# Kernel tuning notes

Hardware: AMD Instinct MI355X
Metric: run time of the kernel (lower is better)

## Reference

```python
import jax, jax.numpy as jnp
import numpy as np

DIM = 1024
HEADS = 16
DIM_HEAD = 64
NB_FEATURES = 266
EPS = 1e-4


def _gaussian_orthogonal_random_matrix(nb_rows, nb_cols, seed=0):
    # Blocks of orthogonal rows (QR of gaussian), rows rescaled by gaussian row norms (scaling=0).
    rng = np.random.default_rng(seed)
    blocks = []
    full, rem = divmod(nb_rows, nb_cols)
    for _ in range(full):
        g = rng.standard_normal((nb_cols, nb_cols))
        q, _ = np.linalg.qr(g)
        blocks.append(q.T)
    if rem > 0:
        g = rng.standard_normal((nb_cols, nb_cols))
        q, _ = np.linalg.qr(g)
        blocks.append(q.T[:rem])
    mat = np.concatenate(blocks, axis=0)
    multiplier = np.linalg.norm(rng.standard_normal((nb_rows, nb_cols)), axis=1)
    return (multiplier[:, None] * mat).astype(np.float32)


def _softmax_kernel(data, proj, is_query):
    # data: [b,h,n,d], proj: [m,d]
    d = data.shape[-1]
    data_normalizer = d ** -0.25
    ratio = proj.shape[0] ** -0.5
    data_dash = jnp.einsum('bhnd,md->bhnm', data * data_normalizer, proj)
    diag = 0.5 * (data_normalizer ** 2) * jnp.sum(data * data, axis=-1, keepdims=True)
    if is_query:
        m = jax.lax.stop_gradient(jnp.max(data_dash, axis=-1, keepdims=True))
    else:
        m = jax.lax.stop_gradient(jnp.max(data_dash, axis=(-1, -2), keepdims=True))
    return ratio * (jnp.exp(data_dash - diag - m) + EPS)


def _linear_attention(q, k, v):
    # q,k: [b,h,n,m], v: [b,h,n,e]
    k_cumsum = jnp.sum(k, axis=-2)                                   # [b,h,m]
    D_inv = 1.0 / jnp.einsum('bhnm,bhm->bhn', q, k_cumsum)           # [b,h,n]
    context = jnp.einsum('bhnm,bhne->bhme', k, v)                    # [b,h,m,e]
    return jnp.einsum('bhme,bhnm,bhn->bhne', context, q, D_inv)      # [b,h,n,e]


def setup_inputs() -> dict:
    key = jax.random.key(0)
    k1, k2, k3, k4, k5 = jax.random.split(key, 5)
    B, N = 2, 4096
    inner = HEADS * DIM_HEAD
    s = DIM ** -0.5
    return {
        'x': jax.random.normal(k1, (B, N, DIM), dtype=jnp.float32),
        'Wq': jax.random.normal(k2, (inner, DIM), dtype=jnp.float32) * s,
        'Wk': jax.random.normal(k3, (inner, DIM), dtype=jnp.float32) * s,
        'Wv': jax.random.normal(k4, (inner, DIM), dtype=jnp.float32) * s,
        'Wo': jax.random.normal(k5, (DIM, inner), dtype=jnp.float32) * s,
        'bo': jnp.zeros((DIM,), dtype=jnp.float32),
        'proj': jnp.asarray(_gaussian_orthogonal_random_matrix(NB_FEATURES, DIM_HEAD)),
    }


def reference(x, Wq, Wk, Wv, Wo, bo, proj):
    b, n, _ = x.shape
    def split_heads(t):
        return t.reshape(b, n, HEADS, DIM_HEAD).transpose(0, 2, 1, 3)  # [b,h,n,d]
    q = split_heads(x @ Wq.T)
    k = split_heads(x @ Wk.T)
    v = split_heads(x @ Wv.T)
    qp = _softmax_kernel(q, proj, is_query=True)
    kp = _softmax_kernel(k, proj, is_query=False)
    out = _linear_attention(qp, kp, v)                                # [b,h,n,d]
    out = out.transpose(0, 2, 1, 3).reshape(b, n, HEADS * DIM_HEAD)
    return out @ Wo.T + bo
```

## Files before the change

kernel.cpp:

```cpp
#include <hip/hip_runtime.h>
#include <hip/hip_bf16.h>
#include <hip/hip_fp16.h>


#define B_   2
#define N_   4096
#define H_   16
#define M_   266
#define MP_  288
#define DIM_ 1024
#define RT_  8192
#define BH_  32
#define LKN  40
#define LSB  296
#define NCH  16

typedef __attribute__((ext_vector_type(8))) short s8v;
typedef __attribute__((ext_vector_type(4))) float f4v;

__device__ __forceinline__ ushort f2bu(float x){ __hip_bfloat16 h = __float2bfloat16(x); return *(ushort*)&h; }

constexpr float NORMC  = 0.35355339059327379f;
constexpr float RATIOC = 0.06131393f;
constexpr float DIAGC  = 0.0625f;
constexpr float EPSC   = 1e-4f;

__device__ __forceinline__ unsigned encf(float x){
    unsigned b = __float_as_uint(x);
    return (b & 0x80000000u) ? ~b : (b | 0x80000000u);
}
__device__ __forceinline__ float decf(unsigned u){
    unsigned b = (u & 0x80000000u) ? (u ^ 0x80000000u) : ~u;
    return __uint_as_float(b);
}

__device__ __forceinline__ void stf(float* p, float v){ *p = v; }
__device__ __forceinline__ void stf(__hip_bfloat16* p, float v){ *p = __float2bfloat16(v); }

__device__ __forceinline__ void gl_lds16(const ushort* g, ushort* l){
    __builtin_amdgcn_global_load_lds(
        (const __attribute__((address_space(1))) unsigned int*)(const unsigned int*)g,
        (__attribute__((address_space(3))) unsigned int*)(unsigned int*)l,
        16, 0, 0);
}

__global__ void cast_x(const float* __restrict__ s, ushort* __restrict__ d){
    const int i = (blockIdx.x * 256 + threadIdx.x) * 8;
    const float4 a = *(const float4*)&s[i];
    const float4 b = *(const float4*)&s[i + 4];
    ushort4 lo, hi;
    lo.x = f2bu(a.x); lo.y = f2bu(a.y); lo.z = f2bu(a.z); lo.w = f2bu(a.w);
    hi.x = f2bu(b.x); hi.y = f2bu(b.y); hi.z = f2bu(b.z); hi.w = f2bu(b.w);
    *(ushort4*)&d[i]     = lo;
    *(ushort4*)&d[i + 4] = hi;
}

__global__ void cast_w(const float* s0, const float* s1, const float* s2, const float* s3,
                       ushort* d0, ushort* d1, ushort* d2, ushort* d3){
    const float* s; ushort* d;
    switch (blockIdx.y) {
        case 0: s = s0; d = d0; break;
        case 1: s = s1; d = d1; break;
        case 2: s = s2; d = d2; break;
        default: s = s3; d = d3; break;
    }
    const int i = (blockIdx.x * 256 + threadIdx.x) * 8;
    const float4 a = *(const float4*)&s[i];
    const float4 b = *(const float4*)&s[i + 4];
    ushort4 lo, hi;
    lo.x = f2bu(a.x); lo.y = f2bu(a.y); lo.z = f2bu(a.z); lo.w = f2bu(a.w);
    hi.x = f2bu(b.x); hi.y = f2bu(b.y); hi.z = f2bu(b.z); hi.w = f2bu(b.w);
    *(ushort4*)&d[i]     = lo;
    *(ushort4*)&d[i + 4] = hi;
}

__global__ void cast_proj(const float* __restrict__ p, ushort* __restrict__ pb){
    const int i = blockIdx.x * 256 + threadIdx.x;
    if (i >= MP_ * 64) return;
    const int m = i >> 6, dc = i & 63;
    pb[i] = f2bu((m < M_) ? NORMC * p[m * 64 + dc] : 0.f);
}

template<bool DIAG, bool BIAS, typename TC>
__launch_bounds__(256)
__global__ void gemm128(const ushort* __restrict__ A, const ushort* __restrict__ Bw,
                        const float* __restrict__ bias, TC* __restrict__ C,
                        float* __restrict__ diag)
{
    __shared__ ushort As[128 * 32];
    __shared__ ushort Bs[128 * 32];

    const int tid  = threadIdx.x;
    const int lane = tid & 63, wave = tid >> 6;
    const int col  = lane & 15, quad = lane >> 4;
    const int wm   = (wave & 1) * 64, wn = (wave >> 1) * 64;
    const int r0   = blockIdx.y * 128, c0 = blockIdx.x * 128;

    const int f0 = tid * 8;
    const int row0 = f0 >> 5, kc0 = f0 & 31;
    const size_t aoff0 = (size_t)(r0 + row0) * DIM_ + kc0;
    const size_t aoff1 = (size_t)(r0 + 64 + row0) * DIM_ + kc0;
    const size_t boff0 = (size_t)(c0 + row0) * DIM_ + kc0;
    const size_t boff1 = (size_t)(c0 + 64 + row0) * DIM_ + kc0;
    ushort* asb0 = &As[wave * 512];
    ushort* asb1 = &As[2048 + wave * 512];
    ushort* bsb0 = &Bs[wave * 512];
    ushort* bsb1 = &Bs[2048 + wave * 512];

    f4v acc[4][4];
    #pragma unroll
    for (int i = 0; i < 4; ++i)
        #pragma unroll
        for (int j = 0; j < 4; ++j) acc[i][j] = (f4v){0.f, 0.f, 0.f, 0.f};

    for (int kk = 0; kk < DIM_; kk += 32) {
        gl_lds16(&A[aoff0 + kk],  asb0);
        gl_lds16(&A[aoff1 + kk],  asb1);
        gl_lds16(&Bw[boff0 + kk], bsb0);
        gl_lds16(&Bw[boff1 + kk], bsb1);
        __syncthreads();
        s8v af[4], bf[4];
        #pragma unroll
        for (int i = 0; i < 4; ++i)
            af[i] = *(const s8v*)&As[(wm + i * 16 + col) * 32 + quad * 8];
        #pragma unroll
        for (int j = 0; j < 4; ++j)
            bf[j] = *(const s8v*)&Bs[(wn + j * 16 + col) * 32 + quad * 8];
        #pragma unroll
        for (int i = 0; i < 4; ++i)
            #pragma unroll
            for (int j = 0; j < 4; ++j)
                acc[i][j] = __builtin_amdgcn_mfma_f32_16x16x32_bf16(af[i], bf[j], acc[i][j], 0, 0, 0);
        __syncthreads();
    }

    float bb[4] = {0.f, 0.f, 0.f, 0.f};
    if (BIAS) {
        #pragma unroll
        for (int j = 0; j < 4; ++j) bb[j] = bias[c0 + wn + j * 16 + col];
    }
    #pragma unroll
    for (int i = 0; i < 4; ++i) {
        #pragma unroll
        for (int r = 0; r < 4; ++r) {
            const size_t grow = (size_t)(r0 + wm + i * 16 + quad * 4 + r);
            #pragma unroll
            for (int j = 0; j < 4; ++j)
                stf(&C[grow * DIM_ + c0 + wn + j * 16 + col], acc[i][j][r] + bb[j]);
        }
    }
    if (DIAG) {
        const int hglob = (c0 + wn) >> 6;
        #pragma unroll
        for (int i = 0; i < 4; ++i) {
            #pragma unroll
            for (int r = 0; r < 4; ++r) {
                float s = 0.f;
                #pragma unroll
                for (int j = 0; j < 4; ++j) s += acc[i][j][r] * acc[i][j][r];
                s += __shfl_xor(s, 1); s += __shfl_xor(s, 2);
                s += __shfl_xor(s, 4); s += __shfl_xor(s, 8);
                if (col == 0)
                    diag[(size_t)(r0 + wm + i * 16 + quad * 4 + r) * H_ + hglob] = DIAGC * s;
            }
        }
    }
}

__launch_bounds__(256)
__global__ void kmax_mfma(const ushort* __restrict__ Kb, const ushort* __restrict__ projb,
                          unsigned* __restrict__ kmaxb)
{
    __shared__ ushort Pl[MP_ * 64];
    __shared__ float wmx[4];
    const int tid  = threadIdx.x;
    const int lane = tid & 63, wave = tid >> 6;
    const int col  = lane & 15, quad = lane >> 4;
    const int bh   = blockIdx.y, b = bh >> 4, h = bh & 15;

    for (int i = tid; i < MP_ * 8; i += 256) {
        const int m = i >> 3, c = i & 7;
        *(uint4*)&Pl[m * 64 + ((c ^ (m & 7)) << 3)] = *(const uint4*)&projb[m * 64 + (c << 3)];
    }
    __syncthreads();

    const int sw0 = (quad ^ (col & 7)) << 3;
    const int sw1 = ((quad | 4) ^ (col & 7)) << 3;

    float mx = -3.4e38f;
    for (int ni = 0; ni < 4; ++ni) {
        const int nb = blockIdx.x * 256 + ni * 64;
        const size_t arow = ((size_t)(b * N_ + nb + wave * 16 + col)) * DIM_ + h * 64 + quad * 8;
        const s8v af0 = *(const s8v*)&Kb[arow];
        const s8v af1 = *(const s8v*)&Kb[arow + 32];
        #pragma unroll
        for (int t = 0; t < 17; ++t) {
            const s8v bf0 = *(const s8v*)&Pl[(t * 16 + col) * 64 + sw0];
            const s8v bf1 = *(const s8v*)&Pl[(t * 16 + col) * 64 + sw1];
            f4v a = (f4v){0.f, 0.f, 0.f, 0.f};
            a = __builtin_amdgcn_mfma_f32_16x16x32_bf16(af0, bf0, a, 0, 0, 0);
            a = __builtin_amdgcn_mfma_f32_16x16x32_bf16(af1, bf1, a, 0, 0, 0);
            if (t * 16 + col < M_) {
                #pragma unroll
                for (int r = 0; r < 4; ++r) mx = fmaxf(mx, a[r]);
            }
        }
    }
    #pragma unroll
    for (int o = 32; o > 0; o >>= 1) mx = fmaxf(mx, __shfl_xor(mx, o));
    if (lane == 0) wmx[wave] = mx;
    __syncthreads();
    if (tid == 0)
        atomicMax(&kmaxb[bh], encf(fmaxf(fmaxf(wmx[0], wmx[1]), fmaxf(wmx[2], wmx[3]))));
}

__launch_bounds__(256)
__global__ void kctx_mfma(const ushort* __restrict__ Kb, const ushort* __restrict__ Vb,
                          const ushort* __restrict__ projb,
                          const float* __restrict__ diagK, const unsigned* __restrict__ kmaxb,
                          float* __restrict__ ctxp, float* __restrict__ kcsp)
{
    __shared__ ushort Pl[MP_ * 64];
    __shared__ ushort Kp[MP_ * LKN];
    __shared__ ushort Vt[64 * LKN];
    __shared__ float kred[2][MP_];

    const int tid  = threadIdx.x;
    const int lane = tid & 63, wave = tid >> 6;
    const int col  = lane & 15, quad = lane >> 4;
    const int bh   = blockIdx.y, b = bh >> 4, h = bh & 15;
    const int n0   = blockIdx.x * (N_ / NCH);
    const float kmax = decf(kmaxb[bh]);
    const int rowblk = wave >> 1;
    const int t0 = (wave & 1) * 9;
    const int t1 = t0 + 9;

    for (int i = tid; i < MP_ * 8; i += 256) {
        const int m = i >> 3, c = i & 7;
        *(uint4*)&Pl[m * 64 + ((c ^ (m & 7)) << 3)] = *(const uint4*)&projb[m * 64 + (c << 3)];
    }
    const int sw0 = (quad ^ (col & 7)) << 3;
    const int sw1 = ((quad | 4) ^ (col & 7)) << 3;

    f4v facc[18];
    #pragma unroll
    for (int t = 0; t < 18; ++t) facc[t] = (f4v){0.f, 0.f, 0.f, 0.f};
    float kcsa[9] = {};

    __syncthreads();

    for (int ks = 0; ks < (N_ / NCH) / 32; ++ks) {
        const int nb = n0 + ks * 32;
        {
            const int n = tid & 31, e0 = (tid >> 5) * 8;
            const s8v vv = *(const s8v*)&Vb[((size_t)(b * N_ + nb + n)) * DIM_ + h * 64 + e0];
            #pragma unroll
            for (int j = 0; j < 8; ++j) Vt[(e0 + j) * LKN + n] = ((const ushort*)&vv)[j];
        }
        const size_t arow = ((size_t)(b * N_ + nb + rowblk * 16 + col)) * DIM_ + h * 64 + quad * 8;
        const s8v af0 = *(const s8v*)&Kb[arow];
        const s8v af1 = *(const s8v*)&Kb[arow + 32];
        float dgr[4];
        #pragma unroll
        for (int r = 0; r < 4; ++r)
            dgr[r] = diagK[((size_t)(b * N_ + nb + rowblk * 16 + quad * 4 + r)) * H_ + h];
        for (int t = t0; t < t1; ++t) {
            const s8v bf0 = *(const s8v*)&Pl[(t * 16 + col) * 64 + sw0];
            const s8v bf1 = *(const s8v*)&Pl[(t * 16 + col) * 64 + sw1];
            f4v a = (f4v){0.f, 0.f, 0.f, 0.f};
            a = __builtin_amdgcn_mfma_f32_16x16x32_bf16(af0, bf0, a, 0, 0, 0);
            a = __builtin_amdgcn_mfma_f32_16x16x32_bf16(af1, bf1, a, 0, 0, 0);
            const int m = t * 16 + col;
            float kp[4];
            #pragma unroll
            for (int r = 0; r < 4; ++r) {
                float v = 0.f;
                if (m < M_) v = RATIOC * (__expf(a[r] - dgr[r] - kmax) + EPSC);
                kp[r] = v;
            }
            kcsa[t - t0] += kp[0] + kp[1] + kp[2] + kp[3];
            ushort4 pk;
            pk.x = f2bu(kp[0]); pk.y = f2bu(kp[1]); pk.z = f2bu(kp[2]); pk.w = f2bu(kp[3]);
            *(ushort4*)&Kp[m * LKN + rowblk * 16 + quad * 4] = pk;
        }
        __syncthreads();
        const s8v bfe = *(const s8v*)&Vt[(wave * 16 + col) * LKN + quad * 8];
        #pragma unroll
        for (int t = 0; t < 18; ++t) {
            const s8v am = *(const s8v*)&Kp[(t * 16 + col) * LKN + quad * 8];
            facc[t] = __builtin_amdgcn_mfma_f32_16x16x32_bf16(am, bfe, facc[t], 0, 0, 0);
        }
        __syncthreads();
    }

    const size_t pbase = ((size_t)bh * NCH + blockIdx.x) * (MP_ * 64);
    #pragma unroll
    for (int t = 0; t < 18; ++t) {
        #pragma unroll
        for (int r = 0; r < 4; ++r)
            ctxp[pbase + (size_t)(t * 16 + quad * 4 + r) * 64 + wave * 16 + col] = facc[t][r];
    }
    for (int t = t0; t < t1; ++t) {
        float s = kcsa[t - t0];
        s += __shfl_xor(s, 16);
        s += __shfl_xor(s, 32);
        if (quad == 0) kred[rowblk][t * 16 + col] = s;
    }
    __syncthreads();
    for (int i = tid; i < MP_; i += 256)
        kcsp[((size_t)bh * NCH + blockIdx.x) * MP_ + i] = kred[0][i] + kred[1][i];
}

__launch_bounds__(256)
__global__ void ctx_reduce(const float* __restrict__ ctxp, const float* __restrict__ kcsp,
                           ushort* __restrict__ ctxT, float* __restrict__ kcs)
{
    const int bh = blockIdx.y, tid = threadIdx.x;
    const int base = blockIdx.x * (MP_ * 64 / 8);
    const size_t cb = (size_t)bh * NCH * (MP_ * 64);
    #pragma unroll
    for (int u = 0; u < 9; ++u) {
        const int flat = base + u * 256 + tid;
        float s = 0.f;
        #pragma unroll
        for (int c = 0; c < NCH; ++c) s += ctxp[cb + (size_t)c * (MP_ * 64) + flat];
        const int m = flat >> 6, e = flat & 63;
        ctxT[((size_t)bh * 64 + e) * MP_ + m] = f2bu(s);
    }
    if (blockIdx.x == 0) {
        for (int i = tid; i < MP_; i += 256) {
            float s = 0.f;
            #pragma unroll
            for (int c = 0; c < NCH; ++c) s += kcsp[((size_t)bh * NCH + c) * MP_ + i];
            kcs[(size_t)bh * MP_ + i] = s;
        }
    }
}

__launch_bounds__(256)
__global__ void qdashout(const ushort* __restrict__ Qb, const ushort* __restrict__ projb,
                         const float* __restrict__ diagQ, const float* __restrict__ kcs,
                         const ushort* __restrict__ ctxT, ushort* __restrict__ Ab)
{
    __shared__ ushort SB[64 * LSB];
    __shared__ float kcl[MP_];
    __shared__ float dinv[64];

    const int tid  = threadIdx.x;
    const int lane = tid & 63, wave = tid >> 6;
    const int col  = lane & 15, quad = lane >> 4;
    const int bh   = blockIdx.y, b = bh >> 4, h = bh & 15;
    const int n0   = blockIdx.x * 64;

    for (int i = tid; i < MP_ * 8; i += 256) {
        const int m = i >> 3, c = i & 7;
        *(uint4*)&SB[m * 64 + ((c ^ (m & 7)) << 3)] = *(const uint4*)&projb[m * 64 + (c << 3)];
    }
    for (int i = tid; i < MP_; i += 256) kcl[i] = kcs[(size_t)bh * MP_ + i];
    __syncthreads();

    const size_t arow = ((size_t)(b * N_ + n0 + wave * 16 + col)) * DIM_ + h * 64 + quad * 8;
    const s8v af0 = *(const s8v*)&Qb[arow];
    const s8v af1 = *(const s8v*)&Qb[arow + 32];
    const int sw0 = (quad ^ (col & 7)) << 3;
    const int sw1 = ((quad | 4) ^ (col & 7)) << 3;

    f4v acc[17];
    #pragma unroll
    for (int t = 0; t < 17; ++t) {
        const s8v bf0 = *(const s8v*)&SB[(t * 16 + col) * 64 + sw0];
        const s8v bf1 = *(const s8v*)&SB[(t * 16 + col) * 64 + sw1];
        f4v a = (f4v){0.f, 0.f, 0.f, 0.f};
        a = __builtin_amdgcn_mfma_f32_16x16x32_bf16(af0, bf0, a, 0, 0, 0);
        a = __builtin_amdgcn_mfma_f32_16x16x32_bf16(af1, bf1, a, 0, 0, 0);
        acc[t] = a;
    }

    float dgr[4], rmx[4];
    #pragma unroll
    for (int r = 0; r < 4; ++r) {
        const int gn = n0 + wave * 16 + quad * 4 + r;
        dgr[r] = diagQ[((size_t)(b * N_ + gn)) * H_ + h];
        float mx = -3.4e38f;
        #pragma unroll
        for (int t = 0; t < 16; ++t) mx = fmaxf(mx, acc[t][r]);
        if (col < 10) mx = fmaxf(mx, acc[16][r]);
        mx = fmaxf(mx, __shfl_xor(mx, 1));
        mx = fmaxf(mx, __shfl_xor(mx, 2));
        mx = fmaxf(mx, __shfl_xor(mx, 4));
        mx = fmaxf(mx, __shfl_xor(mx, 8));
        rmx[r] = mx;
    }

    float den[4] = {0.f, 0.f, 0.f, 0.f};
    #pragma unroll
    for (int t = 0; t < 17; ++t) {
        const int m = t * 16 + col;
        const float kc = kcl[m];
        #pragma unroll
        for (int r = 0; r < 4; ++r) {
            float v = 0.f;
            if (m < M_)
                v = RATIOC * (__expf(acc[t][r] - dgr[r] - rmx[r]) + EPSC);
            acc[t][r] = v;
            den[r] += v * kc;
        }
    }

    __syncthreads();

    #pragma unroll
    for (int r = 0; r < 4; ++r) {
        const int rb = (wave * 16 + quad * 4 + r) * LSB;
        #pragma unroll
        for (int t = 0; t < 17; ++t)
            SB[rb + t * 16 + col] = f2bu(acc[t][r]);
        if (col < 8) *(uint*)&SB[rb + 272 + col * 2] = 0u;
    }
    #pragma unroll
    for (int r = 0; r < 4; ++r) {
        float d = den[r];
        d += __shfl_xor(d, 1); d += __shfl_xor(d, 2);
        d += __shfl_xor(d, 4); d += __shfl_xor(d, 8);
        if (col == 0)
            dinv[wave * 16 + quad * 4 + r] = 1.0f / fmaxf(d, 1e-30f);
    }
    __syncthreads();

    const ushort* ct = ctxT + (size_t)bh * 64 * MP_;
    f4v acc2[4];
    #pragma unroll
    for (int j = 0; j < 4; ++j) acc2[j] = (f4v){0.f, 0.f, 0.f, 0.f};
    #pragma unroll
    for (int kk = 0; kk < 9; ++kk) {
        const s8v afr = *(const s8v*)&SB[(wave * 16 + col) * LSB + kk * 32 + quad * 8];
        #pragma unroll
        for (int j = 0; j < 4; ++j) {
            const s8v bfr = *(const s8v*)&ct[(size_t)(j * 16 + col) * MP_ + kk * 32 + quad * 8];
            acc2[j] = __builtin_amdgcn_mfma_f32_16x16x32_bf16(afr, bfr, acc2[j], 0, 0, 0);
        }
    }
    #pragma unroll
    for (int j = 0; j < 4; ++j) {
        #pragma unroll
        for (int r = 0; r < 4; ++r) {
            const int n = wave * 16 + quad * 4 + r;
            Ab[((size_t)(b * N_ + n0 + n)) * DIM_ + h * 64 + j * 16 + col] =
                f2bu(acc2[j][r] * dinv[n]);
        }
    }
}

extern "C" void kernel_launch(void* const* d_in, const int* in_sizes, int n_in,
                              void* d_out, int out_size, void* d_ws, size_t ws_size,
                              hipStream_t stream)
{
    const float* x    = (const float*)d_in[0];
    const float* Wq   = (const float*)d_in[1];
    const float* Wk   = (const float*)d_in[2];
    const float* Wv   = (const float*)d_in[3];
    const float* Wo   = (const float*)d_in[4];
    const float* bo   = (const float*)d_in[5];
    const float* proj = (const float*)d_in[6];

    char* ws = (char*)d_ws;
    size_t o = 0;
    ushort* xb    = (ushort*)(ws + o); o += (size_t)RT_ * DIM_ * 2;
    ushort* Wqb   = (ushort*)(ws + o); o += (size_t)DIM_ * DIM_ * 2;
    ushort* Wkb   = (ushort*)(ws + o); o += (size_t)DIM_ * DIM_ * 2;
    ushort* Wvb   = (ushort*)(ws + o); o += (size_t)DIM_ * DIM_ * 2;
    ushort* Wob   = (ushort*)(ws + o); o += (size_t)DIM_ * DIM_ * 2;
    ushort* projb = (ushort*)(ws + o); o += (size_t)MP_ * 64 * 2;
    ushort* Qb    = (ushort*)(ws + o); o += (size_t)RT_ * DIM_ * 2;
    ushort* Kb    = (ushort*)(ws + o); o += (size_t)RT_ * DIM_ * 2;
    ushort* Vb    = (ushort*)(ws + o); o += (size_t)RT_ * DIM_ * 2;
    ushort* Ab    = (ushort*)(ws + o); o += (size_t)RT_ * DIM_ * 2;
    float*    ctxp  = (float*)(ws + o);    o += (size_t)BH_ * NCH * MP_ * 64 * 4;
    float*    kcsp  = (float*)(ws + o);    o += (size_t)BH_ * NCH * MP_ * 4;
    float*    kcs   = (float*)(ws + o);    o += (size_t)BH_ * MP_ * 4;
    unsigned* kmaxb = (unsigned*)(ws + o); o += 128;
    float*    diagQ = (float*)(ws + o);    o += (size_t)RT_ * H_ * 4;
    float*    diagK = (float*)(ws + o);    o += (size_t)RT_ * H_ * 4;
    ushort*   ctxT  = (ushort*)(ws + o);   o += (size_t)BH_ * 64 * MP_ * 2;

    hipMemsetAsync(kmaxb, 0, 128, stream);

    cast_x<<<dim3(RT_ * DIM_ / 2048), 256, 0, stream>>>(x, xb);
    cast_w<<<dim3(DIM_ * DIM_ / 2048, 4), 256, 0, stream>>>(Wq, Wk, Wv, Wo, Wqb, Wkb, Wvb, Wob);
    cast_proj<<<dim3(MP_ * 64 / 256), 256, 0, stream>>>(proj, projb);

    const dim3 ggrid(DIM_ / 128, RT_ / 128);
    gemm128<true,  false, __hip_bfloat16><<<ggrid, 256, 0, stream>>>(xb, Wqb, nullptr, (__hip_bfloat16*)Qb, diagQ);
    gemm128<true,  false, __hip_bfloat16><<<ggrid, 256, 0, stream>>>(xb, Wkb, nullptr, (__hip_bfloat16*)Kb, diagK);
    gemm128<false, false, __hip_bfloat16><<<ggrid, 256, 0, stream>>>(xb, Wvb, nullptr, (__hip_bfloat16*)Vb, nullptr);

    kmax_mfma<<<dim3(16, BH_), 256, 0, stream>>>(Kb, projb, kmaxb);
    kctx_mfma<<<dim3(NCH, BH_), 256, 0, stream>>>(Kb, Vb, projb, diagK, kmaxb, ctxp, kcsp);
    ctx_reduce<<<dim3(8, BH_), 256, 0, stream>>>(ctxp, kcsp, ctxT, kcs);
    qdashout<<<dim3(N_ / 64, BH_), 256, 0, stream>>>(Qb, projb, diagQ, kcs, ctxT, Ab);

    gemm128<false, true, float><<<ggrid, 256, 0, stream>>>(Ab, Wob, bo, (float*)d_out, nullptr);
}
```

Baseline: 322.0 us.

## Fuse Q/K/V projections into one GEMM launch and prefetch operands in attention kernels

Replaces the three separate Q, K and V projection GEMMs with a single 24-column-block kernel. It treats the contiguous Wq/Wk/Wv bf16 weights as one 3072-row matrix and routes each column tile to Q, K or V, plus the matching diag buffer. It also adds software prefetching of the next step's K, V and diag registers in kmax_mfma and kctx_mfma. In qdashout it issues the Q and diag loads earlier and double-buffers the ctxT fragment loads in the final MFMA loop. The aim is to cut launch overhead and tail effects, and to hide global-memory latency behind MFMA work. The cost is higher register pressure, and the fused GEMM depends on the weight buffers sitting next to each other in the workspace.

Result: faster. 296.2 us (-8.0%).

```diff
diff --git a/kernel.cpp b/kernel.cpp
--- a/kernel.cpp
+++ b/kernel.cpp
@@ -14,6 +14,7 @@
 #define LKN  40
 #define LSB  296
 #define NCH  16
+#define KS_  8
 
 typedef __attribute__((ext_vector_type(8))) short s8v;
 typedef __attribute__((ext_vector_type(4))) float f4v;
@@ -168,6 +169,92 @@
 }
 
 __launch_bounds__(256)
+__global__ void gemm128_qkv(const ushort* __restrict__ A, const ushort* __restrict__ Bw,
+                            ushort* __restrict__ Q, ushort* __restrict__ K,
+                            ushort* __restrict__ V,
+                            float* __restrict__ diagQ, float* __restrict__ diagK)
+{
+    __shared__ ushort As[128 * 32];
+    __shared__ ushort Bs[128 * 32];
+
+    const int tid  = threadIdx.x;
+    const int lane = tid & 63, wave = tid >> 6;
+    const int col  = lane & 15, quad = lane >> 4;
+    const int wm   = (wave & 1) * 64, wn = (wave >> 1) * 64;
+    const int r0   = blockIdx.y * 128, c0 = blockIdx.x * 128;
+
+    const int f0 = tid * 8;
+    const int row0 = f0 >> 5, kc0 = f0 & 31;
+    const size_t aoff0 = (size_t)(r0 + row0) * DIM_ + kc0;
+    const size_t aoff1 = (size_t)(r0 + 64 + row0) * DIM_ + kc0;
+    const size_t boff0 = (size_t)(c0 + row0) * DIM_ + kc0;
+    const size_t boff1 = (size_t)(c0 + 64 + row0) * DIM_ + kc0;
+    ushort* asb0 = &As[wave * 512];
+    ushort* asb1 = &As[2048 + wave * 512];
+    ushort* bsb0 = &Bs[wave * 512];
+    ushort* bsb1 = &Bs[2048 + wave * 512];
+
+    f4v acc[4][4];
+    #pragma unroll
+    for (int i = 0; i < 4; ++i)
+        #pragma unroll
+        for (int j = 0; j < 4; ++j) acc[i][j] = (f4v){0.f, 0.f, 0.f, 0.f};
+
+    for (int kk = 0; kk < DIM_; kk += 32) {
+        gl_lds16(&A[aoff0 + kk],  asb0);
+        gl_lds16(&A[aoff1 + kk],  asb1);
+        gl_lds16(&Bw[boff0 + kk], bsb0);
+        gl_lds16(&Bw[boff1 + kk], bsb1);
+        __syncthreads();
+        s8v af[4], bf[4];
+        #pragma unroll
+        for (int i = 0; i < 4; ++i)
+            af[i] = *(const s8v*)&As[(wm + i * 16 + col) * 32 + quad * 8];
+        #pragma unroll
+        for (int j = 0; j < 4; ++j)
+            bf[j] = *(const s8v*)&Bs[(wn + j * 16 + col) * 32 + quad * 8];
+        #pragma unroll
+        for (int i = 0; i < 4; ++i)
+            #pragma unroll
+            for (int j = 0; j < 4; ++j)
+                acc[i][j] = __builtin_amdgcn_mfma_f32_16x16x32_bf16(af[i], bf[j], acc[i][j], 0, 0, 0);
+        __syncthreads();
+    }
+
+    const int which = c0 >> 10;
+    const int cc    = c0 & 1023;
+    ushort* C = (which == 0) ? Q : ((which == 1) ? K : V);
+    float* dptr = (which == 0) ? diagQ : ((which == 1) ? diagK : nullptr);
+
+    #pragma unroll
+    for (int i = 0; i < 4; ++i) {
+        #pragma unroll
+        for (int r = 0; r < 4; ++r) {
+            const size_t grow = (size_t)(r0 + wm + i * 16 + quad * 4 + r);
+            #pragma unroll
+            for (int j = 0; j < 4; ++j)
+                C[grow * DIM_ + cc + wn + j * 16 + col] = f2bu(acc[i][j][r]);
+        }
+    }
+    if (dptr) {
+        const int hglob = (cc + wn) >> 6;
+        #pragma unroll
+        for (int i = 0; i < 4; ++i) {
+            #pragma unroll
+            for (int r = 0; r < 4; ++r) {
+                float s = 0.f;
+                #pragma unroll
+                for (int j = 0; j < 4; ++j) s += acc[i][j][r] * acc[i][j][r];
+                s += __shfl_xor(s, 1); s += __shfl_xor(s, 2);
+                s += __shfl_xor(s, 4); s += __shfl_xor(s, 8);
+                if (col == 0)
+                    dptr[(size_t)(r0 + wm + i * 16 + quad * 4 + r) * H_ + hglob] = DIAGC * s;
+            }
+        }
+    }
+}
+
+__launch_bounds__(256)
 __global__ void kmax_mfma(const ushort* __restrict__ Kb, const ushort* __restrict__ projb,
                           unsigned* __restrict__ kmaxb)
 {
@@ -178,6 +265,10 @@
     const int col  = lane & 15, quad = lane >> 4;
     const int bh   = blockIdx.y, b = bh >> 4, h = bh & 15;
 
+    const size_t arowB = ((size_t)(b * N_ + blockIdx.x * 256 + wave * 16 + col)) * DIM_ + h * 64 + quad * 8;
+    s8v aP0 = *(const s8v*)&Kb[arowB];
+    s8v aP1 = *(const s8v*)&Kb[arowB + 32];
+
     for (int i = tid; i < MP_ * 8; i += 256) {
         const int m = i >> 3, c = i & 7;
         *(uint4*)&Pl[m * 64 + ((c ^ (m & 7)) << 3)] = *(const uint4*)&projb[m * 64 + (c << 3)];
@@ -188,11 +279,13 @@
     const int sw1 = ((quad | 4) ^ (col & 7)) << 3;
 
     float mx = -3.4e38f;
+    #pragma unroll
     for (int ni = 0; ni < 4; ++ni) {
-        const int nb = blockIdx.x * 256 + ni * 64;
-        const size_t arow = ((size_t)(b * N_ + nb + wave * 16 + col)) * DIM_ + h * 64 + quad * 8;
-        const s8v af0 = *(const s8v*)&Kb[arow];
-        const s8v af1 = *(const s8v*)&Kb[arow + 32];
+        const s8v af0 = aP0, af1 = aP1;
+        if (ni < 3) {
+            aP0 = *(const s8v*)&Kb[arowB + (size_t)(ni + 1) * 64 * DIM_];
+            aP1 = *(const s8v*)&Kb[arowB + (size_t)(ni + 1) * 64 * DIM_ + 32];
+        }
         #pragma unroll
         for (int t = 0; t < 17; ++t) {
             const s8v bf0 = *(const s8v*)&Pl[(t * 16 + col) * 64 + sw0];
@@ -233,7 +326,16 @@
     const float kmax = decf(kmaxb[bh]);
     const int rowblk = wave >> 1;
     const int t0 = (wave & 1) * 9;
-    const int t1 = t0 + 9;
+
+    const int nst = tid & 31, est = (tid >> 5) * 8;
+    s8v vvP = *(const s8v*)&Vb[((size_t)(b * N_ + n0 + nst)) * DIM_ + h * 64 + est];
+    const size_t arow0 = ((size_t)(b * N_ + n0 + rowblk * 16 + col)) * DIM_ + h * 64 + quad * 8;
+    s8v afP0 = *(const s8v*)&Kb[arow0];
+    s8v afP1 = *(const s8v*)&Kb[arow0 + 32];
+    float dgrP[4];
+    #pragma unroll
+    for (int r = 0; r < 4; ++r)
+        dgrP[r] = diagK[((size_t)(b * N_ + n0 + rowblk * 16 + quad * 4 + r)) * H_ + h];
 
     for (int i = tid; i < MP_ * 8; i += 256) {
         const int m = i >> 3, c = i & 7;
@@ -249,22 +351,16 @@
 
     __syncthreads();
 
-    for (int ks = 0; ks < (N_ / NCH) / 32; ++ks) {
-        const int nb = n0 + ks * 32;
-        {
-            const int n = tid & 31, e0 = (tid >> 5) * 8;
-            const s8v vv = *(const s8v*)&Vb[((size_t)(b * N_ + nb + n)) * DIM_ + h * 64 + e0];
-            #pragma unroll
-            for (int j = 0; j < 8; ++j) Vt[(e0 + j) * LKN + n] = ((const ushort*)&vv)[j];
-        }
-        const size_t arow = ((size_t)(b * N_ + nb + rowblk * 16 + col)) * DIM_ + h * 64 + quad * 8;
-        const s8v af0 = *(const s8v*)&Kb[arow];
-        const s8v af1 = *(const s8v*)&Kb[arow + 32];
+    for (int ks = 0; ks < KS_; ++ks) {
+        const s8v vv = vvP, af0 = afP0, af1 = afP1;
         float dgr[4];
         #pragma unroll
-        for (int r = 0; r < 4; ++r)
-            dgr[r] = diagK[((size_t)(b * N_ + nb + rowblk * 16 + quad * 4 + r)) * H_ + h];
-        for (int t = t0; t < t1; ++t) {
+        for (int r = 0; r < 4; ++r) dgr[r] = dgrP[r];
+
+        #pragma unroll
+        for (int j = 0; j < 8; ++j) Vt[(est + j) * LKN + nst] = ((const ushort*)&vv)[j];
+
+        for (int t = t0; t < t0 + 9; ++t) {
             const s8v bf0 = *(const s8v*)&Pl[(t * 16 + col) * 64 + sw0];
             const s8v bf1 = *(const s8v*)&Pl[(t * 16 + col) * 64 + sw1];
             f4v a = (f4v){0.f, 0.f, 0.f, 0.f};
@@ -283,6 +379,17 @@
             pk.x = f2bu(kp[0]); pk.y = f2bu(kp[1]); pk.z = f2bu(kp[2]); pk.w = f2bu(kp[3]);
             *(ushort4*)&Kp[m * LKN + rowblk * 16 + quad * 4] = pk;
         }
+
+        if (ks + 1 < KS_) {
+            const int nb1 = n0 + (ks + 1) * 32;
+            vvP  = *(const s8v*)&Vb[((size_t)(b * N_ + nb1 + nst)) * DIM_ + h * 64 + est];
+            const size_t arow1 = ((size_t)(b * N_ + nb1 + rowblk * 16 + col)) * DIM_ + h * 64 + quad * 8;
+            afP0 = *(const s8v*)&Kb[arow1];
+            afP1 = *(const s8v*)&Kb[arow1 + 32];
+            #pragma unroll
+            for (int r = 0; r < 4; ++r)
+                dgrP[r] = diagK[((size_t)(b * N_ + nb1 + rowblk * 16 + quad * 4 + r)) * H_ + h];
+        }
         __syncthreads();
         const s8v bfe = *(const s8v*)&Vt[(wave * 16 + col) * LKN + quad * 8];
         #pragma unroll
@@ -300,7 +407,7 @@
         for (int r = 0; r < 4; ++r)
             ctxp[pbase + (size_t)(t * 16 + quad * 4 + r) * 64 + wave * 16 + col] = facc[t][r];
     }
-    for (int t = t0; t < t1; ++t) {
+    for (int t = t0; t < t0 + 9; ++t) {
         float s = kcsa[t - t0];
         s += __shfl_xor(s, 16);
         s += __shfl_xor(s, 32);
@@ -352,6 +459,14 @@
     const int bh   = blockIdx.y, b = bh >> 4, h = bh & 15;
     const int n0   = blockIdx.x * 64;
 
+    const size_t arow = ((size_t)(b * N_ + n0 + wave * 16 + col)) * DIM_ + h * 64 + quad * 8;
+    const s8v af0 = *(const s8v*)&Qb[arow];
+    const s8v af1 = *(const s8v*)&Qb[arow + 32];
+    float dgr[4];
+    #pragma unroll
+    for (int r = 0; r < 4; ++r)
+        dgr[r] = diagQ[((size_t)(b * N_ + n0 + wave * 16 + quad * 4 + r)) * H_ + h];
+
     for (int i = tid; i < MP_ * 8; i += 256) {
         const int m = i >> 3, c = i & 7;
         *(uint4*)&SB[m * 64 + ((c ^ (m & 7)) << 3)] = *(const uint4*)&projb[m * 64 + (c << 3)];
@@ -359,9 +474,6 @@
     for (int i = tid; i < MP_; i += 256) kcl[i] = kcs[(size_t)bh * MP_ + i];
     __syncthreads();
 
-    const size_t arow = ((size_t)(b * N_ + n0 + wave * 16 + col)) * DIM_ + h * 64 + quad * 8;
-    const s8v af0 = *(const s8v*)&Qb[arow];
-    const s8v af1 = *(const s8v*)&Qb[arow + 32];
     const int sw0 = (quad ^ (col & 7)) << 3;
     const int sw1 = ((quad | 4) ^ (col & 7)) << 3;
 
@@ -376,11 +488,9 @@
         acc[t] = a;
     }
 
-    float dgr[4], rmx[4];
+    float rmx[4];
     #pragma unroll
     for (int r = 0; r < 4; ++r) {
-        const int gn = n0 + wave * 16 + quad * 4 + r;
-        dgr[r] = diagQ[((size_t)(b * N_ + gn)) * H_ + h];
         float mx = -3.4e38f;
         #pragma unroll
         for (int t = 0; t < 16; ++t) mx = fmaxf(mx, acc[t][r]);
@@ -407,6 +517,12 @@
         }
     }
 
+    const ushort* ct = ctxT + (size_t)bh * 64 * MP_;
+    s8v bfA[4], bfB[4];
+    #pragma unroll
+    for (int j = 0; j < 4; ++j)
+        bfA[j] = *(const s8v*)&ct[(size_t)(j * 16 + col) * MP_ + quad * 8];
+
     __syncthreads();
 
     #pragma unroll
@@ -427,18 +543,32 @@
     }
     __syncthreads();
 
-    const ushort* ct = ctxT + (size_t)bh * 64 * MP_;
     f4v acc2[4];
     #pragma unroll
     for (int j = 0; j < 4; ++j) acc2[j] = (f4v){0.f, 0.f, 0.f, 0.f};
     #pragma unroll
-    for (int kk = 0; kk < 9; ++kk) {
-        const s8v afr = *(const s8v*)&SB[(wave * 16 + col) * LSB + kk * 32 + quad * 8];
-        #pragma unroll
-        for (int j = 0; j < 4; ++j) {
-            const s8v bfr = *(const s8v*)&ct[(size_t)(j * 16 + col) * MP_ + kk * 32 + quad * 8];
-            acc2[j] = __builtin_amdgcn_mfma_f32_16x16x32_bf16(afr, bfr, acc2[j], 0, 0, 0);
-        }
+    for (int kp = 0; kp < 4; ++kp) {
+        const int k0 = 2 * kp, k1 = 2 * kp + 1, k2 = 2 * kp + 2;
+        #pragma unroll
+        for (int j = 0; j < 4; ++j)
+            bfB[j] = *(const s8v*)&ct[(size_t)(j * 16 + col) * MP_ + k1 * 32 + quad * 8];
+        const s8v afrA = *(const s8v*)&SB[(wave * 16 + col) * LSB + k0 * 32 + quad * 8];
+        #pragma unroll
+        for (int j = 0; j < 4; ++j)
+            acc2[j] = __builtin_amdgcn_mfma_f32_16x16x32_bf16(afrA, bfA[j], acc2[j], 0, 0, 0);
+        #pragma unroll
+        for (int j = 0; j < 4; ++j)
+            bfA[j] = *(const s8v*)&ct[(size_t)(j * 16 + col) * MP_ + k2 * 32 + quad * 8];
+        const s8v afrB = *(const s8v*)&SB[(wave * 16 + col) * LSB + k1 * 32 + quad * 8];
+        #pragma unroll
+        for (int j = 0; j < 4; ++j)
+            acc2[j] = __builtin_amdgcn_mfma_f32_16x16x32_bf16(afrB, bfB[j], acc2[j], 0, 0, 0);
+    }
+    {
+        const s8v afrT = *(const s8v*)&SB[(wave * 16 + col) * LSB + 8 * 32 + quad * 8];
+        #pragma unroll
+        for (int j = 0; j < 4; ++j)
+            acc2[j] = __builtin_amdgcn_mfma_f32_16x16x32_bf16(afrT, bfA[j], acc2[j], 0, 0, 0);
     }
     #pragma unroll
     for (int j = 0; j < 4; ++j) {
@@ -489,15 +619,12 @@
     cast_w<<<dim3(DIM_ * DIM_ / 2048, 4), 256, 0, stream>>>(Wq, Wk, Wv, Wo, Wqb, Wkb, Wvb, Wob);
     cast_proj<<<dim3(MP_ * 64 / 256), 256, 0, stream>>>(proj, projb);
 
-    const dim3 ggrid(DIM_ / 128, RT_ / 128);
-    gemm128<true,  false, __hip_bfloat16><<<ggrid, 256, 0, stream>>>(xb, Wqb, nullptr, (__hip_bfloat16*)Qb, diagQ);
-    gemm128<true,  false, __hip_bfloat16><<<ggrid, 256, 0, stream>>>(xb, Wkb, nullptr, (__hip_bfloat16*)Kb, diagK);
-    gemm128<false, false, __hip_bfloat16><<<ggrid, 256, 0, stream>>>(xb, Wvb, nullptr, (__hip_bfloat16*)Vb, nullptr);
+    gemm128_qkv<<<dim3(24, RT_ / 128), 256, 0, stream>>>(xb, Wqb, Qb, Kb, Vb, diagQ, diagK);
 
     kmax_mfma<<<dim3(16, BH_), 256, 0, stream>>>(Kb, projb, kmaxb);
     kctx_mfma<<<dim3(NCH, BH_), 256, 0, stream>>>(Kb, Vb, projb, diagK, kmaxb, ctxp, kcsp);
     ctx_reduce<<<dim3(8, BH_), 256, 0, stream>>>(ctxp, kcsp, ctxT, kcs);
     qdashout<<<dim3(N_ / 64, BH_), 256, 0, stream>>>(Qb, projb, diagQ, kcs, ctxT, Ab);
 
-    gemm128<false, true, float><<<ggrid, 256, 0, stream>>>(Ab, Wob, bo, (float*)d_out, nullptr);
-}
+    gemm128<false, true, float><<<dim3(DIM_ / 128, RT_ / 128), 256, 0, stream>>>(Ab, Wob, bo, (float*)d_out, nullptr);
+}
```
